# Performance work log

Hardware: AMD Instinct MI355X
Metric: run time of the kernel (lower is better)

The kernel has to match this reference:

```python
import jax, jax.numpy as jnp
import numpy as np

N = 16384          # nodes
E = 262144         # edges (before self-loops)
FIN_N, FIN_E = 768, 64
F, FE = 256, 128   # node/edge channels
H, C = 8, 32       # heads, per-head dim (H*C == F)
L = 2              # num GATv2 modules
NEG_SLOPE = 0.2


def layer_norm(x, g, b, eps=1e-5):
    mu = jnp.mean(x, axis=-1, keepdims=True)
    var = jnp.mean((x - mu) ** 2, axis=-1, keepdims=True)
    return (x - mu) * jax.lax.rsqrt(var + eps) * g + b


def segment_softmax(logits, seg, n):
    # logits: [Et, H], seg: [Et] destination node ids
    m = jax.ops.segment_max(logits, seg, num_segments=n)
    m = jnp.where(jnp.isfinite(m), m, 0.0)
    e = jnp.exp(logits - m[seg])
    s = jax.ops.segment_sum(e, seg, num_segments=n)
    return e / (s[seg] + 1e-16)


def setup_inputs() -> dict:
    key = jax.random.key(0)
    ks = jax.random.split(key, 20)
    inp = {
        "node_feats": jax.random.normal(ks[0], (N, FIN_N), jnp.float32),
        "edge_index": jax.random.randint(ks[1], (2, E), 0, N, dtype=jnp.int32),
        "edge_attr": jax.random.normal(ks[2], (E, FIN_E), jnp.float32),
        # input projections (bias=False)
        "init_node_w": jax.random.normal(ks[3], (F, FIN_N), jnp.float32) * 0.02,
        "init_edge_w": jax.random.normal(ks[4], (FE, FIN_E), jnp.float32) * 0.02,
        # per-layer GATv2 params, stacked on leading layer dim L
        "lin_l_w": jax.random.normal(ks[5], (L, H * C, F), jnp.float32) * 0.05,
        "lin_l_b": jnp.zeros((L, H * C), jnp.float32),
        "lin_r_w": jax.random.normal(ks[6], (L, H * C, F), jnp.float32) * 0.05,
        "lin_r_b": jnp.zeros((L, H * C), jnp.float32),
        "lin_edge_w": jax.random.normal(ks[7], (L, H * C, FE), jnp.float32) * 0.05,
        "att": jax.random.normal(ks[8], (L, H, C), jnp.float32) * 0.05,
        "gat_bias": jnp.zeros((L, H * C), jnp.float32),
        # block params
        "ln1_g": jnp.ones((L, F), jnp.float32), "ln1_b": jnp.zeros((L, F), jnp.float32),
        "mlp_w1": jax.random.normal(ks[9], (L, 2 * F, F), jnp.float32) * 0.05,
        "mlp_w2": jax.random.normal(ks[10], (L, F, 2 * F), jnp.float32) * 0.05,
        "ln2_g": jnp.ones((L, F), jnp.float32), "ln2_b": jnp.zeros((L, F), jnp.float32),
    }
    return inp


def _gatv2_module(x, src, dst, e_emb, p, l, n):
    # e_emb: [Et, H, C] already projected edge embeddings (incl. self-loops)
    x_l = (x @ p["lin_l_w"][l].T + p["lin_l_b"][l]).reshape(n, H, C)
    x_r = (x @ p["lin_r_w"][l].T + p["lin_r_b"][l]).reshape(n, H, C)
    m = x_l[src] + x_r[dst] + e_emb                    # [Et, H, C]
    g = jnp.where(m >= 0, m, NEG_SLOPE * m)            # leaky_relu(0.2)
    logits = jnp.einsum('ehc,hc->eh', g, p["att"][l])
    alpha = segment_softmax(logits, dst, n)            # [Et, H]
    out = jax.ops.segment_sum(alpha[:, :, None] * x_l[src], dst, num_segments=n)
    out = out.reshape(n, H * C) + p["gat_bias"][l]
    # residual -> LN -> MLP -> residual -> LN  (dropout=0, eval mode)
    h = layer_norm(x + out, p["ln1_g"][l], p["ln1_b"][l])
    y = jax.nn.gelu(h @ p["mlp_w1"][l].T, approximate=False) @ p["mlp_w2"][l].T
    return layer_norm(h + y, p["ln2_g"][l], p["ln2_b"][l])


def reference(node_feats, edge_index, edge_attr, init_node_w, init_edge_w,
              lin_l_w, lin_l_b, lin_r_w, lin_r_b, lin_edge_w, att, gat_bias,
              ln1_g, ln1_b, mlp_w1, mlp_w2, ln2_g, ln2_b):
    p = dict(lin_l_w=lin_l_w, lin_l_b=lin_l_b, lin_r_w=lin_r_w, lin_r_b=lin_r_b,
             lin_edge_w=lin_edge_w, att=att, gat_bias=gat_bias, ln1_g=ln1_g,
             ln1_b=ln1_b, mlp_w1=mlp_w1, mlp_w2=mlp_w2, ln2_g=ln2_g, ln2_b=ln2_b)
    x = node_feats @ init_node_w.T                     # [N, F]
    ea = edge_attr @ init_edge_w.T                     # [E, FE]
    src, dst = edge_index[0], edge_index[1]
    # add self loops with fill_value='mean' (mean of incoming edge_attr per node)
    cnt = jax.ops.segment_sum(jnp.ones((E,), ea.dtype), dst, num_segments=N)
    loop_attr = jax.ops.segment_sum(ea, dst, num_segments=N) / jnp.maximum(cnt, 1.0)[:, None]
    ea_all = jnp.concatenate([ea, loop_attr], axis=0)  # [E+N, FE]
    ar = jnp.arange(N, dtype=src.dtype)
    src_all = jnp.concatenate([src, ar])
    dst_all = jnp.concatenate([dst, ar])
    for l in range(L):
        e_emb = (ea_all @ lin_edge_w[l].T).reshape(-1, H, C)
        x = _gatv2_module(x, src_all, dst_all, e_emb, p, l, N)
    return x
```

## Files before the change

kernel.cpp:

```cpp
#include <hip/hip_runtime.h>

typedef unsigned short u16;
typedef __attribute__((ext_vector_type(8))) short s8v;
typedef __attribute__((ext_vector_type(4))) float f4v;

#define NN 16384
#define EE 262144
#define ET (EE + NN)
#define NTILES (ET / 64)

__device__ __forceinline__ float bfu(u16 h){ return __uint_as_float((unsigned)h << 16); }
__device__ __forceinline__ u16 f2bf(float f){
  unsigned u = __float_as_uint(f);
  unsigned r = u + 0x7FFFu + ((u >> 16) & 1u);
  return (u16)(r >> 16);
}
__device__ __forceinline__ float ldf(const void* p, size_t i, int isbf){
  return isbf ? bfu(((const u16*)p)[i]) : ((const float*)p)[i];
}
__device__ __forceinline__ float gelu_f(float x){ return 0.5f*x*(1.0f+erff(x*0.7071067811865475f)); }

__device__ __forceinline__ uint4 load8bf(const void* p, size_t eoff, int isbf){
  if (isbf) return *(const uint4*)((const u16*)p + eoff);
  const float* f = (const float*)p + eoff;
  uint4 r;
  r.x = (unsigned)f2bf(f[0]) | ((unsigned)f2bf(f[1])<<16);
  r.y = (unsigned)f2bf(f[2]) | ((unsigned)f2bf(f[3])<<16);
  r.z = (unsigned)f2bf(f[4]) | ((unsigned)f2bf(f[5])<<16);
  r.w = (unsigned)f2bf(f[6]) | ((unsigned)f2bf(f[7])<<16);
  return r;
}

__global__ void k_detect(const void* nf, int* flag)
{
  int t = threadIdx.x;
  const float* f = (const float*)nf;
  int cnt = 0;
  for (int i = t; i < 4096; i += 256) {
    float a = fabsf(f[i]);
    if (a > 1e-5f && a < 100.0f) cnt++;
  }
  __shared__ int s[256];
  s[t] = cnt; __syncthreads();
  for (int st = 128; st > 0; st >>= 1) { if (t < st) s[t] += s[t+st]; __syncthreads(); }
  if (t == 0) *flag = (s[0] < 2048) ? 1 : 0;
}

template<int ACT, int CFMT>
__global__ __launch_bounds__(256)
void mfma_gemm(const void* __restrict__ A, int a_fmt,
               const void* __restrict__ B1, size_t b1off,
               const void* __restrict__ B2, size_t b2off, int nsplit,
               const void* __restrict__ bias1, const void* __restrict__ bias2,
               size_t bioff, int has_bias,
               void* __restrict__ C, int M, int N, int K,
               const int* __restrict__ dflag)
{
  int isbf = *dflag;
  int af = (a_fmt == 2) ? isbf : a_fmt;
  __shared__ u16 As[128*40];
  __shared__ u16 Bs[128*40];
  int bm = blockIdx.y*128, bn = blockIdx.x*128;
  int t = threadIdx.x;
  int w = t>>6, lane = t&63, l4 = lane&15, quad = lane>>4;
  int wm = w>>1, wn = w&1;
  f4v zero = {0.f,0.f,0.f,0.f};
  f4v acc[4][4];
  #pragma unroll
  for (int i=0;i<4;i++)
    #pragma unroll
    for (int j=0;j<4;j++) acc[i][j] = zero;

  for (int k0 = 0; k0 < K; k0 += 32) {
    __syncthreads();
    #pragma unroll
    for (int it = 0; it < 2; ++it) {
      int sid = t + it*256;
      int row = sid >> 2, sk = sid & 3;
      *(uint4*)&As[row*40 + sk*8] = load8bf(A, (size_t)(bm+row)*K + k0 + sk*8, af);
      int col = bn + row;
      uint4 vb;
      if (col < nsplit) vb = load8bf(B1, b1off + (size_t)col*K + k0 + sk*8, isbf);
      else              vb = load8bf(B2, b2off + (size_t)(col-nsplit)*K + k0 + sk*8, isbf);
      *(uint4*)&Bs[row*40 + sk*8] = vb;
    }
    __syncthreads();
    s8v a[4], b[4];
    #pragma unroll
    for (int i=0;i<4;i++) a[i] = *(const s8v*)&As[(wm*64 + i*16 + l4)*40 + quad*8];
    #pragma unroll
    for (int j=0;j<4;j++) b[j] = *(const s8v*)&Bs[(wn*64 + j*16 + l4)*40 + quad*8];
    #pragma unroll
    for (int i=0;i<4;i++)
      #pragma unroll
      for (int j=0;j<4;j++)
        acc[i][j] = __builtin_amdgcn_mfma_f32_16x16x32_bf16(a[i], b[j], acc[i][j], 0,0,0);
  }
  #pragma unroll
  for (int i=0;i<4;i++)
    #pragma unroll
    for (int j=0;j<4;j++) {
      int col = bn + wn*64 + j*16 + l4;
      float bv = 0.f;
      if (has_bias) bv = (col < nsplit) ? ldf(bias1, bioff + col, isbf)
                                        : ldf(bias2, bioff + col - nsplit, isbf);
      #pragma unroll
      for (int r=0;r<4;r++) {
        int row = bm + wm*64 + i*16 + quad*4 + r;
        float v = acc[i][j][r] + bv;
        if (ACT==1) v = gelu_f(v);
        if (CFMT==1) ((u16*)C)[(size_t)row*N + col] = f2bf(v);
        else         ((float*)C)[(size_t)row*N + col] = v;
      }
    }
}

__global__ void k_count(const int* __restrict__ dst, int* __restrict__ deg)
{
  int e = blockIdx.x*256 + threadIdx.x;
  if (e >= ET) return;
  int d = (e < EE) ? dst[e] : (e - EE);
  atomicAdd(&deg[d], 1);
}

__global__ void k_scan(const int* __restrict__ deg, int* __restrict__ rowstart)
{
  __shared__ int csum[256];
  int t = threadIdx.x;
  int s = 0;
  for (int i=0;i<64;i++) s += deg[t*64+i];
  csum[t] = s;
  __syncthreads();
  if (t == 0) {
    int r = 0;
    for (int i=0;i<256;i++){ int v = csum[i]; csum[i] = r; r += v; }
    rowstart[NN] = r;
  }
  __syncthreads();
  int b = csum[t];
  for (int i=0;i<64;i++){ rowstart[t*64+i] = b; b += deg[t*64+i]; }
}

__global__ void k_scatter(const int* __restrict__ src, const int* __restrict__ dst,
                          const int* __restrict__ rowstart,
                          int* __restrict__ fill, int* __restrict__ csr,
                          int* __restrict__ srcc, int* __restrict__ dstc)
{
  int e = blockIdx.x*256 + threadIdx.x;
  if (e >= ET) return;
  int d  = (e < EE) ? dst[e] : (e - EE);
  int sv = (e < EE) ? src[e] : (e - EE);
  int pos = rowstart[d] + atomicAdd(&fill[d], 1);
  csr[pos]  = e;
  srcc[pos] = sv;
  dstc[pos] = d;
}

__global__ void k_loopmean(const int* __restrict__ csr, const int* __restrict__ rowstart,
                           const void* __restrict__ edge_attr, u16* __restrict__ loopmean,
                           const int* __restrict__ dflag)
{
  int isbf = *dflag;
  int n = blockIdx.x, j = threadIdx.x;
  int s = rowstart[n], e1 = rowstart[n+1];
  float sum = 0.f; int cnt = 0;
  for (int p = s; p < e1; ++p) {
    int eid = csr[p];
    if (eid < EE) { sum += ldf(edge_attr, (size_t)eid*64 + j, isbf); cnt++; }
  }
  loopmean[(size_t)n*64 + j] = f2bf(sum / (float)max(cnt, 1));
}

__global__ void k_wc(const void* __restrict__ We, const void* __restrict__ iew,
                     u16* __restrict__ Wcb, const int* __restrict__ dflag)
{
  int isbf = *dflag;
  int idx = blockIdx.x*256 + threadIdx.x;
  int j = idx & 63, c = (idx >> 6) & 255, l = idx >> 14;
  float s = 0.f;
  for (int k=0;k<128;k++) s += ldf(We, ((size_t)l*256 + c)*128 + k, isbf) * ldf(iew, (size_t)k*64 + j, isbf);
  Wcb[idx] = f2bf(s);
}

__global__ __launch_bounds__(256)
void k_elogits(const int* __restrict__ csr, const int* __restrict__ srcc, const int* __restrict__ dstc,
               const u16* __restrict__ Wcb, const u16* __restrict__ xlr,
               const void* __restrict__ edge_attr, const u16* __restrict__ loopmean,
               const void* __restrict__ att, size_t att_off,
               float* __restrict__ logits, const int* __restrict__ dflag)
{
  int isbf = *dflag;
  __shared__ u16 WcF[32*64*8];
  __shared__ u16 attr_s[64*72];
  __shared__ float satt[256];
  __shared__ int ssrc[64], sdst[64];

  int t = threadIdx.x;
  int w = t>>6, lane = t&63, l4 = lane&15, quad = lane>>4;

  satt[t] = ldf(att, att_off + t, isbf);
  #pragma unroll
  for (int f = 0; f < 8; ++f) {
    int fr = w + f*4;
    int i = fr >> 1, ks = fr & 1;
    *(uint4*)&WcF[(fr*64 + lane)*8] = *(const uint4*)&Wcb[(size_t)(16*i + l4)*64 + ks*32 + quad*8];
  }

  f4v zero = {0.f,0.f,0.f,0.f};
  for (int tile = blockIdx.x; tile < NTILES; tile += gridDim.x) {
    int e0 = tile*64;
    __syncthreads();
    if (t < 64) {
      ssrc[t] = srcc[e0 + t];
      sdst[t] = dstc[e0 + t];
    }
    {
      int er = t >> 2, part = t & 3;
      int eid = csr[e0 + er];
      uint4 v0, v1;
      if (eid < EE) {
        v0 = load8bf(edge_attr, (size_t)eid*64 + part*16,     isbf);
        v1 = load8bf(edge_attr, (size_t)eid*64 + part*16 + 8, isbf);
      } else {
        v0 = *(const uint4*)&loopmean[(size_t)(eid-EE)*64 + part*16];
        v1 = *(const uint4*)&loopmean[(size_t)(eid-EE)*64 + part*16 + 8];
      }
      *(uint4*)&attr_s[er*72 + part*16]     = v0;
      *(uint4*)&attr_s[er*72 + part*16 + 8] = v1;
    }
    __syncthreads();

    s8v b0 = *(const s8v*)&attr_s[(w*16 + l4)*72 + quad*8];
    s8v b1 = *(const s8v*)&attr_s[(w*16 + l4)*72 + 32 + quad*8];
    f4v acc[16];
    #pragma unroll
    for (int i=0;i<16;++i){
      s8v a0 = *(const s8v*)&WcF[((2*i  )*64 + lane)*8];
      s8v a1 = *(const s8v*)&WcF[((2*i+1)*64 + lane)*8];
      acc[i] = __builtin_amdgcn_mfma_f32_16x16x32_bf16(a0, b0, zero, 0,0,0);
      acc[i] = __builtin_amdgcn_mfma_f32_16x16x32_bf16(a1, b1, acc[i], 0,0,0);
    }

    int me = w*16 + l4;
    int sn = ssrc[me], dn = sdst[me];
    float ph[8] = {0.f,0.f,0.f,0.f,0.f,0.f,0.f,0.f};
    #pragma unroll
    for (int i=0;i<16;++i){
      uint2 xlv = *(const uint2*)&xlr[(size_t)sn*512 +       i*16 + quad*4];
      uint2 xrv = *(const uint2*)&xlr[(size_t)dn*512 + 256 + i*16 + quad*4];
      float4 av = *(const float4*)&satt[i*16 + quad*4];
      float m0 = acc[i][0] + bfu((u16)(xlv.x & 0xffff)) + bfu((u16)(xrv.x & 0xffff));
      float m1 = acc[i][1] + bfu((u16)(xlv.x >> 16))    + bfu((u16)(xrv.x >> 16));
      float m2 = acc[i][2] + bfu((u16)(xlv.y & 0xffff)) + bfu((u16)(xrv.y & 0xffff));
      float m3 = acc[i][3] + bfu((u16)(xlv.y >> 16))    + bfu((u16)(xrv.y >> 16));
      float g0 = fmaxf(m0, 0.2f*m0), g1 = fmaxf(m1, 0.2f*m1);
      float g2 = fmaxf(m2, 0.2f*m2), g3 = fmaxf(m3, 0.2f*m3);
      ph[i>>1] += av.x*g0 + av.y*g1 + av.z*g2 + av.w*g3;
    }
    #pragma unroll
    for (int h=0;h<8;++h){
      ph[h] += __shfl_xor(ph[h], 16);
      ph[h] += __shfl_xor(ph[h], 32);
    }
    if (quad == 0){
      float4 lo = {ph[0], ph[1], ph[2], ph[3]};
      float4 hi = {ph[4], ph[5], ph[6], ph[7]};
      *(float4*)&logits[(size_t)(e0 + me)*8]     = lo;
      *(float4*)&logits[(size_t)(e0 + me)*8 + 4] = hi;
    }
  }
}

__global__ __launch_bounds__(256)
void k_aggln(const int* __restrict__ srcc, const int* __restrict__ rowstart,
             const float* __restrict__ logits, const u16* __restrict__ xlr, const float* __restrict__ xbuf,
             const void* __restrict__ gat_bias, const void* __restrict__ ln1g, const void* __restrict__ ln1b,
             size_t poff, float* __restrict__ hbuf, const int* __restrict__ dflag)
{
  int isbf = *dflag;
  int lane = threadIdx.x & 63, wid = threadIdx.x >> 6;
  int n = blockIdx.x*4 + wid;
  int s = rowstart[n], deg = rowstart[n+1] - s;
  int myh = lane >> 3;
  float mrun = -3.0e38f, lrun = 0.f;
  float a0=0.f, a1=0.f, a2=0.f, a3=0.f;

  for (int c0 = 0; c0 < deg; c0 += 64) {
    int idx = s + c0 + lane; if (idx >= ET) idx = ET-1;
    int sv = srcc[idx];
    int lim = min(64, deg - c0);
    size_t lbase = (size_t)(s + c0)*8 + myh;
    for (int j = 0; j < lim; ++j) {
      int sn  = __shfl(sv, j);
      float lg = logits[lbase + (size_t)j*8];
      uint2 xv = *(const uint2*)&xlr[(size_t)sn*512 + 4*lane];
      float mn = fmaxf(mrun, lg);
      float sc = __expf(mrun - mn);
      float wv = __expf(lg - mn);
      mrun = mn;
      lrun = lrun*sc + wv;
      a0 = a0*sc + wv*bfu((u16)(xv.x & 0xffff));
      a1 = a1*sc + wv*bfu((u16)(xv.x >> 16));
      a2 = a2*sc + wv*bfu((u16)(xv.y & 0xffff));
      a3 = a3*sc + wv*bfu((u16)(xv.y >> 16));
    }
  }
  float inv = 1.f/(lrun + 1e-16f);
  int c = 4*lane;
  float4 res = *(const float4*)&xbuf[(size_t)n*256 + c];
  float o0 = a0*inv + ldf(gat_bias, poff+c+0, isbf) + res.x;
  float o1 = a1*inv + ldf(gat_bias, poff+c+1, isbf) + res.y;
  float o2 = a2*inv + ldf(gat_bias, poff+c+2, isbf) + res.z;
  float o3 = a3*inv + ldf(gat_bias, poff+c+3, isbf) + res.w;

  float v = o0+o1+o2+o3;
  #pragma unroll
  for (int off=1; off<64; off<<=1) v += __shfl_xor(v, off);
  float mu = v * (1.f/256.f);
  float d0=o0-mu, d1=o1-mu, d2=o2-mu, d3=o3-mu;
  float v2 = d0*d0+d1*d1+d2*d2+d3*d3;
  #pragma unroll
  for (int off=1; off<64; off<<=1) v2 += __shfl_xor(v2, off);
  float wn = rsqrtf(v2*(1.f/256.f) + 1e-5f);
  float4 outv;
  outv.x = d0*wn*ldf(ln1g, poff+c+0, isbf) + ldf(ln1b, poff+c+0, isbf);
  outv.y = d1*wn*ldf(ln1g, poff+c+1, isbf) + ldf(ln1b, poff+c+1, isbf);
  outv.z = d2*wn*ldf(ln1g, poff+c+2, isbf) + ldf(ln1b, poff+c+2, isbf);
  outv.w = d3*wn*ldf(ln1g, poff+c+3, isbf) + ldf(ln1b, poff+c+3, isbf);
  *(float4*)&hbuf[(size_t)n*256 + c] = outv;
}

__global__ __launch_bounds__(256)
void k_ln_add(const float* __restrict__ a, const u16* __restrict__ b2,
              const void* __restrict__ gg, const void* __restrict__ bb, size_t poff,
              float* __restrict__ out, const int* __restrict__ dflag)
{
  int isbf = *dflag;
  int n = blockIdx.x, t = threadIdx.x;
  __shared__ float r[256];
  float x = a[(size_t)n*256 + t] + bfu(b2[(size_t)n*256 + t]);
  r[t] = x; __syncthreads();
  for (int st = 128; st > 0; st >>= 1) { if (t < st) r[t] += r[t+st]; __syncthreads(); }
  float mu = r[0] * (1.f/256.f);
  __syncthreads();
  float d = x - mu;
  r[t] = d*d; __syncthreads();
  for (int st = 128; st > 0; st >>= 1) { if (t < st) r[t] += r[t+st]; __syncthreads(); }
  float var = r[0] * (1.f/256.f);
  out[(size_t)n*256 + t] = d * rsqrtf(var + 1e-5f) * ldf(gg, poff + t, isbf) + ldf(bb, poff + t, isbf);
}

__global__ void k_out(const float* __restrict__ x, void* __restrict__ out, const int* __restrict__ dflag)
{
  int isbf = *dflag;
  int i = blockIdx.x*256 + threadIdx.x;
  if (isbf) ((u16*)out)[i] = f2bf(x[i]);
  else      ((float*)out)[i] = x[i];
}

extern "C" void kernel_launch(void* const* d_in, const int* in_sizes, int n_in,
                              void* d_out, int out_size, void* d_ws, size_t ws_size,
                              hipStream_t stream)
{
  const void* node_feats = d_in[0];
  const int*  edge_index = (const int*)d_in[1];
  const void* edge_attr  = d_in[2];
  const void* init_node_w= d_in[3];
  const void* init_edge_w= d_in[4];
  const void* lin_l_w    = d_in[5];
  const void* lin_l_b    = d_in[6];
  const void* lin_r_w    = d_in[7];
  const void* lin_r_b    = d_in[8];
  const void* lin_edge_w = d_in[9];
  const void* att        = d_in[10];
  const void* gat_bias   = d_in[11];
  const void* ln1_g      = d_in[12];
  const void* ln1_b      = d_in[13];
  const void* mlp_w1     = d_in[14];
  const void* mlp_w2     = d_in[15];
  const void* ln2_g      = d_in[16];
  const void* ln2_b      = d_in[17];

  const int* srcp = edge_index;
  const int* dstp = edge_index + EE;

  char* p = (char*)d_ws;
  auto alloc = [&](size_t bytes) { void* r = (void*)p; p += (bytes + 255) & ~(size_t)255; return r; };
  int*   dflag   = (int*)alloc(256);
  int*   deg     = (int*)alloc((size_t)NN*4);
  int*   rowstart= (int*)alloc((size_t)(NN+1)*4);
  int*   fill    = (int*)alloc((size_t)NN*4);
  int*   csr     = (int*)alloc((size_t)ET*4);
  int*   srcc    = (int*)alloc((size_t)ET*4);
  int*   dstc    = (int*)alloc((size_t)ET*4);
  u16*   Wcb     = (u16*)alloc((size_t)2*256*64*2);
  u16*   loopmean= (u16*)alloc((size_t)NN*64*2);
  float* logits  = (float*)alloc((size_t)ET*8*4);
  float* xbuf    = (float*)alloc((size_t)NN*256*4);
  float* hbuf    = (float*)alloc((size_t)NN*256*4);
  u16*   xlr     = (u16*)alloc((size_t)NN*512*2);
  u16*   ymid    = xlr;
  u16*   y2      = (u16*)d_out;

  hipMemsetAsync(deg,  0, (size_t)NN*4, stream);
  hipMemsetAsync(fill, 0, (size_t)NN*4, stream);

  k_detect <<<1, 256, 0, stream>>>(node_feats, dflag);

  k_count  <<<(ET+255)/256, 256, 0, stream>>>(dstp, deg);
  k_scan   <<<1, 256, 0, stream>>>(deg, rowstart);
  k_scatter<<<(ET+255)/256, 256, 0, stream>>>(srcp, dstp, rowstart, fill, csr, srcc, dstc);
  k_loopmean<<<NN, 64, 0, stream>>>(csr, rowstart, edge_attr, loopmean, dflag);
  k_wc     <<<128, 256, 0, stream>>>(lin_edge_w, init_edge_w, Wcb, dflag);

  mfma_gemm<0,0><<<dim3(2,128), 256, 0, stream>>>(node_feats, 2, init_node_w, 0, init_node_w, 0, 1<<29,
                                                  nullptr, nullptr, 0, 0, xbuf, NN, 256, 768, dflag);

  for (int l = 0; l < 2; ++l) {
    size_t wo = (size_t)l*256*256;
    size_t bo = (size_t)l*256;
    mfma_gemm<0,1><<<dim3(4,128), 256, 0, stream>>>(xbuf, 0, lin_l_w, wo, lin_r_w, wo, 256,
                                                    lin_l_b, lin_r_b, bo, 1, xlr, NN, 512, 256, dflag);
    k_elogits<<<768, 256, 0, stream>>>(csr, srcc, dstc, Wcb + (size_t)l*256*64, xlr,
                                       edge_attr, loopmean, att, (size_t)l*256, logits, dflag);
    k_aggln<<<NN/4, 256, 0, stream>>>(srcc, rowstart, logits, xlr, xbuf,
                                      gat_bias, ln1_g, ln1_b, bo, hbuf, dflag);
    mfma_gemm<1,1><<<dim3(4,128), 256, 0, stream>>>(hbuf, 0, mlp_w1, (size_t)l*512*256, mlp_w1, 0, 1<<29,
                                                    nullptr, nullptr, 0, 0, ymid, NN, 512, 256, dflag);
    mfma_gemm<0,1><<<dim3(2,128), 256, 0, stream>>>(ymid, 1, mlp_w2, (size_t)l*256*512, mlp_w2, 0, 1<<29,
                                                    nullptr, nullptr, 0, 0, y2, NN, 256, 512, dflag);
    k_ln_add<<<NN, 256, 0, stream>>>(hbuf, y2, ln2_g, ln2_b, bo, xbuf, dflag);
  }

  k_out<<<(NN*256)/256, 256, 0, stream>>>(xbuf, d_out, dflag);
}
```

Measured before the change: 735.3 us.

## Replace tiled GEMM with full-K LDS A-panel kernel and bf16 activation copies

The generic 128x128 K-tiled GEMM is replaced by a kernel that loads the whole K-width A row panel into swizzled LDS once. Each wave then streams its B columns straight from global memory, with no per-K-step LDS staging or barriers. Producers (aggln, ln_add, the init GEMM) now also write bf16 copies of their activations so the GEMMs read half-size inputs without converting. Node features get a separate conversion pass into scratch space that aliases the logits buffer. The trade-offs are extra bf16 writes and more global B traffic, since B is no longer reused through LDS across the M tile.

```diff
diff --git a/kernel.cpp b/kernel.cpp
--- a/kernel.cpp
+++ b/kernel.cpp
@@ -46,71 +46,104 @@
   if (t == 0) *flag = (s[0] < 2048) ? 1 : 0;
 }
 
-template<int ACT, int CFMT>
+__global__ void k_cvt(const void* __restrict__ in, u16* __restrict__ out, const int* __restrict__ dflag)
+{
+  int isbf = *dflag;
+  size_t i = ((size_t)blockIdx.x*256 + threadIdx.x)*8;
+  *(uint4*)&out[i] = load8bf(in, i, isbf);
+}
+
+template<int KK, int MF, int ACT, int CFMT>
 __global__ __launch_bounds__(256)
-void mfma_gemm(const void* __restrict__ A, int a_fmt,
-               const void* __restrict__ B1, size_t b1off,
-               const void* __restrict__ B2, size_t b2off, int nsplit,
-               const void* __restrict__ bias1, const void* __restrict__ bias2,
-               size_t bioff, int has_bias,
-               void* __restrict__ C, int M, int N, int K,
-               const int* __restrict__ dflag)
-{
-  int isbf = *dflag;
-  int af = (a_fmt == 2) ? isbf : a_fmt;
-  __shared__ u16 As[128*40];
-  __shared__ u16 Bs[128*40];
-  int bm = blockIdx.y*128, bn = blockIdx.x*128;
+void mg2(const u16* __restrict__ A,
+         const void* __restrict__ B1, size_t b1off,
+         const void* __restrict__ B2, size_t b2off, int nsplit,
+         const void* __restrict__ bias1, const void* __restrict__ bias2,
+         size_t bioff, int has_bias,
+         void* __restrict__ C, void* __restrict__ C2, int N,
+         const int* __restrict__ dflag)
+{
+  constexpr int ROWS = MF*16;
+  constexpr int CPR  = KK/8;
+  constexpr int IT   = ROWS*CPR/256;
+  __shared__ u16 As[ROWS*KK];
+
+  int isbf = *dflag;
   int t = threadIdx.x;
   int w = t>>6, lane = t&63, l4 = lane&15, quad = lane>>4;
-  int wm = w>>1, wn = w&1;
+  int bm = blockIdx.y*ROWS, bn = blockIdx.x*256;
+
+  const u16* Abase = A + (size_t)bm*KK;
+  uint4 stg[IT];
+  #pragma unroll
+  for (int it=0; it<IT; ++it) {
+    int c = it*256 + t;
+    int gc = c ^ ((c/CPR)&7);
+    stg[it] = *(const uint4*)(Abase + (size_t)gc*8);
+  }
+  #pragma unroll
+  for (int it=0; it<IT; ++it) {
+    int c = it*256 + t;
+    *(uint4*)((char*)As + (size_t)c*16) = stg[it];
+  }
+  __syncthreads();
+
+  const void* Bp[4]; size_t Be[4]; int colj[4];
+  #pragma unroll
+  for (int j=0;j<4;++j) {
+    int cj = bn + w*64 + j*16 + l4;
+    colj[j] = cj;
+    if (cj < nsplit) { Bp[j] = B1; Be[j] = b1off + (size_t)cj*KK; }
+    else             { Bp[j] = B2; Be[j] = b2off + (size_t)(cj-nsplit)*KK; }
+  }
+
   f4v zero = {0.f,0.f,0.f,0.f};
-  f4v acc[4][4];
-  #pragma unroll
-  for (int i=0;i<4;i++)
+  f4v acc[MF][4];
+  #pragma unroll
+  for (int i=0;i<MF;i++)
     #pragma unroll
     for (int j=0;j<4;j++) acc[i][j] = zero;
 
-  for (int k0 = 0; k0 < K; k0 += 32) {
-    __syncthreads();
-    #pragma unroll
-    for (int it = 0; it < 2; ++it) {
-      int sid = t + it*256;
-      int row = sid >> 2, sk = sid & 3;
-      *(uint4*)&As[row*40 + sk*8] = load8bf(A, (size_t)(bm+row)*K + k0 + sk*8, af);
-      int col = bn + row;
-      uint4 vb;
-      if (col < nsplit) vb = load8bf(B1, b1off + (size_t)col*K + k0 + sk*8, isbf);
-      else              vb = load8bf(B2, b2off + (size_t)(col-nsplit)*K + k0 + sk*8, isbf);
-      *(uint4*)&Bs[row*40 + sk*8] = vb;
-    }
-    __syncthreads();
-    s8v a[4], b[4];
-    #pragma unroll
-    for (int i=0;i<4;i++) a[i] = *(const s8v*)&As[(wm*64 + i*16 + l4)*40 + quad*8];
-    #pragma unroll
-    for (int j=0;j<4;j++) b[j] = *(const s8v*)&Bs[(wn*64 + j*16 + l4)*40 + quad*8];
-    #pragma unroll
-    for (int i=0;i<4;i++)
+  #pragma unroll
+  for (int s=0; s<KK/32; ++s) {
+    s8v b[4];
+    #pragma unroll
+    for (int j=0;j<4;++j) {
+      uint4 bv = load8bf(Bp[j], Be[j] + s*32 + quad*8, isbf);
+      b[j] = *(s8v*)&bv;
+    }
+    s8v a[MF];
+    #pragma unroll
+    for (int i=0;i<MF;++i) {
+      int row = i*16 + l4;
+      int byte = (row*(KK*2) + s*64 + quad*16) ^ ((row&7)<<4);
+      a[i] = *(const s8v*)((const char*)As + byte);
+    }
+    #pragma unroll
+    for (int i=0;i<MF;++i)
       #pragma unroll
-      for (int j=0;j<4;j++)
+      for (int j=0;j<4;++j)
         acc[i][j] = __builtin_amdgcn_mfma_f32_16x16x32_bf16(a[i], b[j], acc[i][j], 0,0,0);
   }
-  #pragma unroll
-  for (int i=0;i<4;i++)
-    #pragma unroll
-    for (int j=0;j<4;j++) {
-      int col = bn + wn*64 + j*16 + l4;
-      float bv = 0.f;
-      if (has_bias) bv = (col < nsplit) ? ldf(bias1, bioff + col, isbf)
-                                        : ldf(bias2, bioff + col - nsplit, isbf);
+
+  #pragma unroll
+  for (int i=0;i<MF;++i)
+    #pragma unroll
+    for (int j=0;j<4;++j) {
+      int cj = colj[j];
+      float bvs = 0.f;
+      if (has_bias) bvs = (cj < nsplit) ? ldf(bias1, bioff + cj, isbf)
+                                        : ldf(bias2, bioff + cj - nsplit, isbf);
       #pragma unroll
-      for (int r=0;r<4;r++) {
-        int row = bm + wm*64 + i*16 + quad*4 + r;
-        float v = acc[i][j][r] + bv;
+      for (int r=0;r<4;++r) {
+        int row = bm + i*16 + quad*4 + r;
+        float v = acc[i][j][r] + bvs;
         if (ACT==1) v = gelu_f(v);
-        if (CFMT==1) ((u16*)C)[(size_t)row*N + col] = f2bf(v);
-        else         ((float*)C)[(size_t)row*N + col] = v;
+        if (CFMT==1) ((u16*)C)[(size_t)row*N + cj] = f2bf(v);
+        else {
+          ((float*)C)[(size_t)row*N + cj] = v;
+          if (CFMT==2) ((u16*)C2)[(size_t)row*N + cj] = f2bf(v);
+        }
       }
     }
 }
@@ -275,7 +308,7 @@
 void k_aggln(const int* __restrict__ srcc, const int* __restrict__ rowstart,
              const float* __restrict__ logits, const u16* __restrict__ xlr, const float* __restrict__ xbuf,
              const void* __restrict__ gat_bias, const void* __restrict__ ln1g, const void* __restrict__ ln1b,
-             size_t poff, float* __restrict__ hbuf, const int* __restrict__ dflag)
+             size_t poff, float* __restrict__ hbuf, u16* __restrict__ hbufb, const int* __restrict__ dflag)
 {
   int isbf = *dflag;
   int lane = threadIdx.x & 63, wid = threadIdx.x >> 6;
@@ -328,12 +361,16 @@
   outv.z = d2*wn*ldf(ln1g, poff+c+2, isbf) + ldf(ln1b, poff+c+2, isbf);
   outv.w = d3*wn*ldf(ln1g, poff+c+3, isbf) + ldf(ln1b, poff+c+3, isbf);
   *(float4*)&hbuf[(size_t)n*256 + c] = outv;
+  uint2 hb;
+  hb.x = (unsigned)f2bf(outv.x) | ((unsigned)f2bf(outv.y)<<16);
+  hb.y = (unsigned)f2bf(outv.z) | ((unsigned)f2bf(outv.w)<<16);
+  *(uint2*)&hbufb[(size_t)n*256 + c] = hb;
 }
 
 __global__ __launch_bounds__(256)
 void k_ln_add(const float* __restrict__ a, const u16* __restrict__ b2,
               const void* __restrict__ gg, const void* __restrict__ bb, size_t poff,
-              float* __restrict__ out, const int* __restrict__ dflag)
+              float* __restrict__ out, u16* __restrict__ outb, const int* __restrict__ dflag)
 {
   int isbf = *dflag;
   int n = blockIdx.x, t = threadIdx.x;
@@ -347,7 +384,9 @@
   r[t] = d*d; __syncthreads();
   for (int st = 128; st > 0; st >>= 1) { if (t < st) r[t] += r[t+st]; __syncthreads(); }
   float var = r[0] * (1.f/256.f);
-  out[(size_t)n*256 + t] = d * rsqrtf(var + 1e-5f) * ldf(gg, poff + t, isbf) + ldf(bb, poff + t, isbf);
+  float o = d * rsqrtf(var + 1e-5f) * ldf(gg, poff + t, isbf) + ldf(bb, poff + t, isbf);
+  out[(size_t)n*256 + t] = o;
+  outb[(size_t)n*256 + t] = f2bf(o);
 }
 
 __global__ void k_out(const float* __restrict__ x, void* __restrict__ out, const int* __restrict__ dflag)
@@ -396,9 +435,12 @@
   u16*   Wcb     = (u16*)alloc((size_t)2*256*64*2);
   u16*   loopmean= (u16*)alloc((size_t)NN*64*2);
   float* logits  = (float*)alloc((size_t)ET*8*4);
+  float* hbuf    = (float*)alloc((size_t)NN*256*4);
   float* xbuf    = (float*)alloc((size_t)NN*256*4);
-  float* hbuf    = (float*)alloc((size_t)NN*256*4);
+  u16*   xbufb   = (u16*)alloc((size_t)NN*256*2);
+  u16*   hbufb   = (u16*)alloc((size_t)NN*256*2);
   u16*   xlr     = (u16*)alloc((size_t)NN*512*2);
+  u16*   nfb     = (u16*)logits;
   u16*   ymid    = xlr;
   u16*   y2      = (u16*)d_out;
 
@@ -413,23 +455,24 @@
   k_loopmean<<<NN, 64, 0, stream>>>(csr, rowstart, edge_attr, loopmean, dflag);
   k_wc     <<<128, 256, 0, stream>>>(lin_edge_w, init_edge_w, Wcb, dflag);
 
-  mfma_gemm<0,0><<<dim3(2,128), 256, 0, stream>>>(node_feats, 2, init_node_w, 0, init_node_w, 0, 1<<29,
-                                                  nullptr, nullptr, 0, 0, xbuf, NN, 256, 768, dflag);
+  k_cvt<<<(NN*768)/(8*256), 256, 0, stream>>>(node_feats, nfb, dflag);
+  mg2<768,2,0,2><<<dim3(1, NN/32), 256, 0, stream>>>(nfb, init_node_w, 0, init_node_w, 0, 1<<29,
+                                                     nullptr, nullptr, 0, 0, xbuf, xbufb, 256, dflag);
 
   for (int l = 0; l < 2; ++l) {
     size_t wo = (size_t)l*256*256;
     size_t bo = (size_t)l*256;
-    mfma_gemm<0,1><<<dim3(4,128), 256, 0, stream>>>(xbuf, 0, lin_l_w, wo, lin_r_w, wo, 256,
-                                                    lin_l_b, lin_r_b, bo, 1, xlr, NN, 512, 256, dflag);
+    mg2<256,4,0,1><<<dim3(2, NN/64), 256, 0, stream>>>(xbufb, lin_l_w, wo, lin_r_w, wo, 256,
+                                                       lin_l_b, lin_r_b, bo, 1, xlr, nullptr, 512, dflag);
     k_elogits<<<768, 256, 0, stream>>>(csr, srcc, dstc, Wcb + (size_t)l*256*64, xlr,
                                        edge_attr, loopmean, att, (size_t)l*256, logits, dflag);
     k_aggln<<<NN/4, 256, 0, stream>>>(srcc, rowstart, logits, xlr, xbuf,
-                                      gat_bias, ln1_g, ln1_b, bo, hbuf, dflag);
-    mfma_gemm<1,1><<<dim3(4,128), 256, 0, stream>>>(hbuf, 0, mlp_w1, (size_t)l*512*256, mlp_w1, 0, 1<<29,
-                                                    nullptr, nullptr, 0, 0, ymid, NN, 512, 256, dflag);
-    mfma_gemm<0,1><<<dim3(2,128), 256, 0, stream>>>(ymid, 1, mlp_w2, (size_t)l*256*512, mlp_w2, 0, 1<<29,
-                                                    nullptr, nullptr, 0, 0, y2, NN, 256, 512, dflag);
-    k_ln_add<<<NN, 256, 0, stream>>>(hbuf, y2, ln2_g, ln2_b, bo, xbuf, dflag);
+                                      gat_bias, ln1_g, ln1_b, bo, hbuf, hbufb, dflag);
+    mg2<256,4,1,1><<<dim3(2, NN/64), 256, 0, stream>>>(hbufb, mlp_w1, (size_t)l*512*256, mlp_w1, 0, 1<<29,
+                                                       nullptr, nullptr, 0, 0, ymid, nullptr, 512, dflag);
+    mg2<512,4,0,1><<<dim3(1, NN/64), 256, 0, stream>>>(ymid, mlp_w2, (size_t)l*256*512, mlp_w2, 0, 1<<29,
+                                                       nullptr, nullptr, 0, 0, y2, nullptr, 256, dflag);
+    k_ln_add<<<NN, 256, 0, stream>>>(hbuf, y2, ln2_g, ln2_b, bo, xbuf, xbufb, dflag);
   }
 
   k_out<<<(NN*256)/256, 256, 0, stream>>>(xbuf, d_out, dflag);
```

New measurement: 982.8 us. 1.34x slower.
